# Kernel optimization log

Hardware: AMD Instinct MI355X
Metric: run time of the kernel (lower is better)

The kernel has to match this reference:

```python
import jax, jax.numpy as jnp
import numpy as np

I = 512  # input_size
H = 512  # hidden_size
L = 512  # sequence length
N = 64   # batch


def setup_inputs() -> dict:
    key = jax.random.key(0)
    ks = jax.random.split(key, 12)
    s_ih = 1.0 / np.sqrt(H)
    inp = {
        "input": jax.random.normal(ks[0], (L, N, I), dtype=jnp.float32),
        "h_0": jax.random.normal(ks[1], (2, N, H), dtype=jnp.float32),
        # layer 0 params
        "W_ih_l0": jax.random.uniform(ks[2], (H, I), jnp.float32, -s_ih, s_ih),
        "W_hh_l0": jax.random.uniform(ks[3], (H, H), jnp.float32, -s_ih, s_ih),
        "b_ih_l0": jax.random.uniform(ks[4], (H,), jnp.float32, -s_ih, s_ih),
        "b_hh_l0": jax.random.uniform(ks[5], (H,), jnp.float32, -s_ih, s_ih),
        # layer 1 params (input is layer 0 hidden state, size H)
        "W_ih_l1": jax.random.uniform(ks[6], (H, H), jnp.float32, -s_ih, s_ih),
        "W_hh_l1": jax.random.uniform(ks[7], (H, H), jnp.float32, -s_ih, s_ih),
        "b_ih_l1": jax.random.uniform(ks[8], (H,), jnp.float32, -s_ih, s_ih),
        "b_hh_l1": jax.random.uniform(ks[9], (H,), jnp.float32, -s_ih, s_ih),
    }
    return inp


def reference(input, h_0, W_ih_l0, W_hh_l0, b_ih_l0, b_hh_l0,
              W_ih_l1, W_hh_l1, b_ih_l1, b_hh_l1):
    """2-layer Elman RNN with tanh: h[t] = tanh(x[t] W_ih^T + b_ih + h[t-1] W_hh^T + b_hh).
    Layer 1 consumes layer 0's hidden state at the same timestep.
    Returns (output: (L, N, H), h_n: (2, N, H)).
    """

    def step(carry, x_t):
        h0, h1 = carry  # each (N, H)
        h0_new = jnp.tanh(x_t @ W_ih_l0.T + b_ih_l0 + h0 @ W_hh_l0.T + b_hh_l0)
        h1_new = jnp.tanh(h0_new @ W_ih_l1.T + b_ih_l1 + h1 @ W_hh_l1.T + b_hh_l1)
        return (h0_new, h1_new), h1_new

    (h0_n, h1_n), output = jax.lax.scan(step, (h_0[0], h_0[1]), input)
    h_n = jnp.stack([h0_n, h1_n], axis=0)
    return output, h_n
```

## Files before the change

kernel.cpp:

```cpp
#include <hip/hip_runtime.h>
#include <hip/hip_bf16.h>
#include <math.h>

#define L_SEQ 512
#define N_B   64
#define H_D   512
#define M_TOT (L_SEQ * N_B)

typedef unsigned short u16;
typedef unsigned long long u64;
typedef __attribute__((ext_vector_type(8))) short short8;
typedef __attribute__((ext_vector_type(4))) float f32x4;
typedef __attribute__((ext_vector_type(4))) int i32x4;
typedef __attribute__((ext_vector_type(2))) int i32x2;

__device__ __forceinline__ u16 f2bf(float f) {
    unsigned int u = __builtin_bit_cast(unsigned int, f);
    u = u + 0x7fffu + ((u >> 16) & 1u);
    return (u16)(u >> 16);
}

__device__ __forceinline__ float fast_tanh(float x) {
    float e = __expf(2.0f * x);
    return 1.0f - 2.0f / (e + 1.0f);
}

__device__ __forceinline__ void st_h(u16* p, u16 v) {
    __hip_atomic_store(p, v, __ATOMIC_RELAXED, __HIP_MEMORY_SCOPE_AGENT);
}
__device__ __forceinline__ void st_flag(int* p, int v) {
    __hip_atomic_store(p, v, __ATOMIC_RELAXED, __HIP_MEMORY_SCOPE_AGENT);
}

#define LD16(f, p)                                                          \
  asm volatile(                                                             \
    "global_load_dwordx4 %0, %16, off\n\t"                                  \
    "global_load_dwordx4 %1, %16, off offset:64\n\t"                        \
    "global_load_dwordx4 %2, %16, off offset:128\n\t"                       \
    "global_load_dwordx4 %3, %16, off offset:192\n\t"                       \
    "global_load_dwordx4 %4, %16, off offset:256\n\t"                       \
    "global_load_dwordx4 %5, %16, off offset:320\n\t"                       \
    "global_load_dwordx4 %6, %16, off offset:384\n\t"                       \
    "global_load_dwordx4 %7, %16, off offset:448\n\t"                       \
    "global_load_dwordx4 %8, %16, off offset:512\n\t"                       \
    "global_load_dwordx4 %9, %16, off offset:576\n\t"                       \
    "global_load_dwordx4 %10, %16, off offset:640\n\t"                      \
    "global_load_dwordx4 %11, %16, off offset:704\n\t"                      \
    "global_load_dwordx4 %12, %16, off offset:768\n\t"                      \
    "global_load_dwordx4 %13, %16, off offset:832\n\t"                      \
    "global_load_dwordx4 %14, %16, off offset:896\n\t"                      \
    "global_load_dwordx4 %15, %16, off offset:960\n\t"                      \
    "s_waitcnt vmcnt(0)"                                                    \
    : "=&v"(f[0]), "=&v"(f[1]), "=&v"(f[2]), "=&v"(f[3]),                   \
      "=&v"(f[4]), "=&v"(f[5]), "=&v"(f[6]), "=&v"(f[7]),                   \
      "=&v"(f[8]), "=&v"(f[9]), "=&v"(f[10]), "=&v"(f[11]),                 \
      "=&v"(f[12]), "=&v"(f[13]), "=&v"(f[14]), "=&v"(f[15])                \
    : "v"(p) : "memory")

#define LD16X2(f, g, p0, p1)                                                \
  asm volatile(                                                             \
    "global_load_dwordx4 %0, %32, off\n\t"                                  \
    "global_load_dwordx4 %16, %33, off\n\t"                                 \
    "global_load_dwordx4 %1, %32, off offset:64\n\t"                        \
    "global_load_dwordx4 %17, %33, off offset:64\n\t"                       \
    "global_load_dwordx4 %2, %32, off offset:128\n\t"                       \
    "global_load_dwordx4 %18, %33, off offset:128\n\t"                      \
    "global_load_dwordx4 %3, %32, off offset:192\n\t"                       \
    "global_load_dwordx4 %19, %33, off offset:192\n\t"                      \
    "global_load_dwordx4 %4, %32, off offset:256\n\t"                       \
    "global_load_dwordx4 %20, %33, off offset:256\n\t"                      \
    "global_load_dwordx4 %5, %32, off offset:320\n\t"                       \
    "global_load_dwordx4 %21, %33, off offset:320\n\t"                      \
    "global_load_dwordx4 %6, %32, off offset:384\n\t"                       \
    "global_load_dwordx4 %22, %33, off offset:384\n\t"                      \
    "global_load_dwordx4 %7, %32, off offset:448\n\t"                       \
    "global_load_dwordx4 %23, %33, off offset:448\n\t"                      \
    "global_load_dwordx4 %8, %32, off offset:512\n\t"                       \
    "global_load_dwordx4 %24, %33, off offset:512\n\t"                      \
    "global_load_dwordx4 %9, %32, off offset:576\n\t"                       \
    "global_load_dwordx4 %25, %33, off offset:576\n\t"                      \
    "global_load_dwordx4 %10, %32, off offset:640\n\t"                      \
    "global_load_dwordx4 %26, %33, off offset:640\n\t"                      \
    "global_load_dwordx4 %11, %32, off offset:704\n\t"                      \
    "global_load_dwordx4 %27, %33, off offset:704\n\t"                      \
    "global_load_dwordx4 %12, %32, off offset:768\n\t"                      \
    "global_load_dwordx4 %28, %33, off offset:768\n\t"                      \
    "global_load_dwordx4 %13, %32, off offset:832\n\t"                      \
    "global_load_dwordx4 %29, %33, off offset:832\n\t"                      \
    "global_load_dwordx4 %14, %32, off offset:896\n\t"                      \
    "global_load_dwordx4 %30, %33, off offset:896\n\t"                      \
    "global_load_dwordx4 %15, %32, off offset:960\n\t"                      \
    "global_load_dwordx4 %31, %33, off offset:960\n\t"                      \
    "s_waitcnt vmcnt(0)"                                                    \
    : "=&v"(f[0]), "=&v"(f[1]), "=&v"(f[2]), "=&v"(f[3]),                   \
      "=&v"(f[4]), "=&v"(f[5]), "=&v"(f[6]), "=&v"(f[7]),                   \
      "=&v"(f[8]), "=&v"(f[9]), "=&v"(f[10]), "=&v"(f[11]),                 \
      "=&v"(f[12]), "=&v"(f[13]), "=&v"(f[14]), "=&v"(f[15]),               \
      "=&v"(g[0]), "=&v"(g[1]), "=&v"(g[2]), "=&v"(g[3]),                   \
      "=&v"(g[4]), "=&v"(g[5]), "=&v"(g[6]), "=&v"(g[7]),                   \
      "=&v"(g[8]), "=&v"(g[9]), "=&v"(g[10]), "=&v"(g[11]),                 \
      "=&v"(g[12]), "=&v"(g[13]), "=&v"(g[14]), "=&v"(g[15])                \
    : "v"(p0), "v"(p1) : "memory")

#define WAITVM asm volatile("s_waitcnt vmcnt(0)" ::: "memory")

__global__ void k_prep(const float* __restrict__ x,
                       const float* __restrict__ w0ih, const float* __restrict__ w0hh,
                       const float* __restrict__ b0i,  const float* __restrict__ b0h,
                       const float* __restrict__ w1ih, const float* __restrict__ w1hh,
                       const float* __restrict__ b1i,  const float* __restrict__ b1h,
                       u16* __restrict__ xb,
                       u16* __restrict__ w0ihb, u16* __restrict__ w0hhb,
                       u16* __restrict__ w1ihb, u16* __restrict__ w1hhb,
                       float* __restrict__ bias0, float* __restrict__ bias1,
                       int* __restrict__ flags)
{
    const int stride = gridDim.x * blockDim.x;
    const int tid = blockIdx.x * blockDim.x + threadIdx.x;
    for (int i = tid; i < M_TOT * H_D / 4; i += stride) {
        const float4 v = ((const float4*)x)[i];
        ushort4 o;
        o.x = f2bf(v.x); o.y = f2bf(v.y); o.z = f2bf(v.z); o.w = f2bf(v.w);
        ((ushort4*)xb)[i] = o;
    }
    for (int i = tid; i < H_D * H_D; i += stride) {
        w0ihb[i] = f2bf(w0ih[i]);
        w0hhb[i] = f2bf(w0hh[i]);
        w1ihb[i] = f2bf(w1ih[i]);
        w1hhb[i] = f2bf(w1hh[i]);
    }
    if (tid < H_D) {
        bias0[tid] = b0i[tid] + b0h[tid];
        bias1[tid] = b1i[tid] + b1h[tid];
    }
    if (tid < 192) flags[tid] = 0;
}

__global__ __launch_bounds__(256)
void k_gemm(const u16* __restrict__ A, const u16* __restrict__ W,
            const float* __restrict__ bias, float* __restrict__ out)
{
    __shared__ u16 As[128][40];
    __shared__ u16 Ws[128][40];
    const int m0 = blockIdx.x * 128;
    const int n0 = blockIdx.y * 128;
    const int tid = threadIdx.x;
    const int w = tid >> 6, l = tid & 63, q = l >> 4, lr = l & 15;
    const int mw = (w >> 1) * 64, nw = (w & 1) * 64;
    const int skg = (tid & 3) * 8;
    const int smr = tid >> 2;

    f32x4 acc[4][4];
    #pragma unroll
    for (int i = 0; i < 4; ++i)
        #pragma unroll
        for (int j = 0; j < 4; ++j)
            acc[i][j] = (f32x4){0.f, 0.f, 0.f, 0.f};

    for (int kk = 0; kk < H_D; kk += 32) {
        *(uint4*)&As[smr][skg]      = *(const uint4*)(A + (size_t)(m0 + smr) * H_D + kk + skg);
        *(uint4*)&As[smr + 64][skg] = *(const uint4*)(A + (size_t)(m0 + smr + 64) * H_D + kk + skg);
        *(uint4*)&Ws[smr][skg]      = *(const uint4*)(W + (size_t)(n0 + smr) * H_D + kk + skg);
        *(uint4*)&Ws[smr + 64][skg] = *(const uint4*)(W + (size_t)(n0 + smr + 64) * H_D + kk + skg);
        __syncthreads();
        short8 af[4], bf[4];
        #pragma unroll
        for (int rt = 0; rt < 4; ++rt) af[rt] = *(const short8*)&As[mw + rt*16 + lr][q*8];
        #pragma unroll
        for (int nt = 0; nt < 4; ++nt) bf[nt] = *(const short8*)&Ws[nw + nt*16 + lr][q*8];
        #pragma unroll
        for (int rt = 0; rt < 4; ++rt)
            #pragma unroll
            for (int nt = 0; nt < 4; ++nt)
                acc[rt][nt] = __builtin_amdgcn_mfma_f32_16x16x32_bf16(af[rt], bf[nt], acc[rt][nt], 0, 0, 0);
        __syncthreads();
    }
    #pragma unroll
    for (int nt = 0; nt < 4; ++nt) {
        const int col = n0 + nw + nt*16 + lr;
        const float bv = bias[col];
        #pragma unroll
        for (int rt = 0; rt < 4; ++rt) {
            #pragma unroll
            for (int r = 0; r < 4; ++r) {
                const int row = m0 + mw + rt*16 + q*4 + r;
                out[(size_t)row * H_D + col] = acc[rt][nt][r] + bv;
            }
        }
    }
}

__global__ __launch_bounds__(256, 1)
void k_rec_fused(const u16* __restrict__ Whh0, const u16* __restrict__ Wih1,
                 const u16* __restrict__ Whh1,
                 const float* __restrict__ h_init,
                 const float* __restrict__ pre0,
                 const float* __restrict__ bias1,
                 u16* __restrict__ h0buf, u16* __restrict__ h1buf,
                 float* __restrict__ out, float* __restrict__ hn,
                 int* __restrict__ flags0, int* __restrict__ flags1)
{
    (void)__hip_atomic_load(flags0, __ATOMIC_ACQUIRE, __HIP_MEMORY_SCOPE_AGENT);

    const int tid = threadIdx.x;
    const int w = tid >> 6, l = tid & 63, q = l >> 4, lr = l & 15;
    const int r0 = w * 16;
    const int m = r0 + lr;

    if (blockIdx.x < 16) {
        const int c = blockIdx.x;
        const int nbase = c * 32;
        short8 breg[16][2];
        #pragma unroll
        for (int kt = 0; kt < 16; ++kt)
            #pragma unroll
            for (int nt = 0; nt < 2; ++nt)
                breg[kt][nt] = *(const short8*)(Whh0 + (size_t)(nbase + nt*16 + lr) * H_D + kt*32 + q*8);

        #pragma unroll
        for (int j = 0; j < 8; ++j) {
            int idx = l * 8 + j;
            int row = r0 + (idx >> 5);
            int col = nbase + (idx & 31);
            st_h(h0buf + (size_t)row * H_D + col, f2bf(h_init[row * H_D + col]));
        }
        WAITVM;
        __syncthreads();
        if (tid == 0) st_flag(flags0 + c, 1);

        for (int t = 0; t < L_SEQ; ++t) {
            const float* pt = pre0 + (size_t)t * (N_B * H_D)
                            + (size_t)(r0 + lr) * H_D + nbase + q*4;
            f32x4 acc0a = *(const f32x4*)pt;
            f32x4 acc1a = *(const f32x4*)(pt + 16);
            f32x4 acc0b = (f32x4){0.f,0.f,0.f,0.f};
            f32x4 acc1b = (f32x4){0.f,0.f,0.f,0.f};

            if (w == 0) {
                const int* p = flags0 + (l & 15);
                while (true) {
                    int v = __hip_atomic_load(p, __ATOMIC_RELAXED, __HIP_MEMORY_SCOPE_AGENT);
                    if (__all(v >= t + 1)) break;
                    __builtin_amdgcn_s_sleep(1);
                }
                asm volatile("" ::: "memory");
            }
            __syncthreads();

            const u16* hs = h0buf + ((size_t)t * N_B + m) * H_D + q*8;
            i32x4 f[16];
            LD16(f, hs);
            #pragma unroll
            for (int kt = 0; kt < 16; kt += 2) {
                acc0a = __builtin_amdgcn_mfma_f32_16x16x32_bf16(breg[kt][0],   __builtin_bit_cast(short8, f[kt]),   acc0a, 0, 0, 0);
                acc1a = __builtin_amdgcn_mfma_f32_16x16x32_bf16(breg[kt][1],   __builtin_bit_cast(short8, f[kt]),   acc1a, 0, 0, 0);
                acc0b = __builtin_amdgcn_mfma_f32_16x16x32_bf16(breg[kt+1][0], __builtin_bit_cast(short8, f[kt+1]), acc0b, 0, 0, 0);
                acc1b = __builtin_amdgcn_mfma_f32_16x16x32_bf16(breg[kt+1][1], __builtin_bit_cast(short8, f[kt+1]), acc1b, 0, 0, 0);
            }
            float v0[4], v1[4];
            #pragma unroll
            for (int r = 0; r < 4; ++r) {
                v0[r] = fast_tanh(acc0a[r] + acc0b[r]);
                v1[r] = fast_tanh(acc1a[r] + acc1b[r]);
            }
            i32x2 d0, d1;
            d0[0] = (int)((unsigned)f2bf(v0[0]) | ((unsigned)f2bf(v0[1]) << 16));
            d0[1] = (int)((unsigned)f2bf(v0[2]) | ((unsigned)f2bf(v0[3]) << 16));
            d1[0] = (int)((unsigned)f2bf(v1[0]) | ((unsigned)f2bf(v1[1]) << 16));
            d1[1] = (int)((unsigned)f2bf(v1[2]) | ((unsigned)f2bf(v1[3]) << 16));
            u16* hd = h0buf + (size_t)(t+1) * (N_B * H_D)
                    + (size_t)(r0 + lr) * H_D + nbase + q*4;
            asm volatile(
                "global_store_dwordx2 %2, %0, off sc1\n\t"
                "global_store_dwordx2 %2, %1, off offset:32 sc1"
                :: "v"(d0), "v"(d1), "v"(hd) : "memory");
            WAITVM;
            __syncthreads();
            if (tid == 0) st_flag(flags0 + c, t + 2);

            if (t == L_SEQ - 1) {
                f32x4 o0 = {v0[0], v0[1], v0[2], v0[3]};
                f32x4 o1 = {v1[0], v1[1], v1[2], v1[3]};
                *(f32x4*)(hn + (size_t)(r0 + lr) * H_D + nbase + q*4)      = o0;
                *(f32x4*)(hn + (size_t)(r0 + lr) * H_D + nbase + 16 + q*4) = o1;
            }
        }
    } else {
        const int c = blockIdx.x - 16;
        const int nbase = c * 16;
        short8 bregI[16], bregH[16];
        #pragma unroll
        for (int kt = 0; kt < 16; ++kt) {
            bregI[kt] = *(const short8*)(Wih1 + (size_t)(nbase + lr) * H_D + kt*32 + q*8);
            bregH[kt] = *(const short8*)(Whh1 + (size_t)(nbase + lr) * H_D + kt*32 + q*8);
        }
        const f32x4 bv4 = *(const f32x4*)(bias1 + nbase + q*4);

        const float* hi1 = h_init + N_B * H_D;
        #pragma unroll
        for (int j = 0; j < 4; ++j) {
            int idx = l * 4 + j;
            int row = r0 + (idx >> 4);
            int col = nbase + (idx & 15);
            st_h(h1buf + (size_t)row * H_D + col, f2bf(hi1[row * H_D + col]));
        }
        WAITVM;
        __syncthreads();
        if (tid == 0) st_flag(flags1 + c, 1);

        for (int t = 0; t < L_SEQ; ++t) {
            if (w == 0) {
                const int* p;
                int need;
                if (l < 16)      { p = flags0 + l;        need = t + 2; }
                else if (l < 48) { p = flags1 + (l - 16); need = t + 1; }
                else             { p = flags0;            need = 0;     }
                while (true) {
                    int v = __hip_atomic_load(p, __ATOMIC_RELAXED, __HIP_MEMORY_SCOPE_AGENT);
                    if (__all(v >= need)) break;
                    __builtin_amdgcn_s_sleep(1);
                }
                asm volatile("" ::: "memory");
            }
            __syncthreads();

            const u16* p0 = h0buf + ((size_t)(t+1) * N_B + m) * H_D + q*8;
            const u16* p1 = h1buf + ((size_t)t     * N_B + m) * H_D + q*8;
            i32x4 f[16], g[16];
            LD16X2(f, g, p0, p1);
            f32x4 accA = bv4;
            f32x4 accB = (f32x4){0.f,0.f,0.f,0.f};
            f32x4 accC = (f32x4){0.f,0.f,0.f,0.f};
            f32x4 accD = (f32x4){0.f,0.f,0.f,0.f};
            #pragma unroll
            for (int kt = 0; kt < 16; kt += 2) {
                accA = __builtin_amdgcn_mfma_f32_16x16x32_bf16(bregI[kt],   __builtin_bit_cast(short8, f[kt]),   accA, 0, 0, 0);
                accB = __builtin_amdgcn_mfma_f32_16x16x32_bf16(bregH[kt],   __builtin_bit_cast(short8, g[kt]),   accB, 0, 0, 0);
                accC = __builtin_amdgcn_mfma_f32_16x16x32_bf16(bregI[kt+1], __builtin_bit_cast(short8, f[kt+1]), accC, 0, 0, 0);
                accD = __builtin_amdgcn_mfma_f32_16x16x32_bf16(bregH[kt+1], __builtin_bit_cast(short8, g[kt+1]), accD, 0, 0, 0);
            }
            float v[4];
            #pragma unroll
            for (int r = 0; r < 4; ++r)
                v[r] = fast_tanh(accA[r] + accB[r] + accC[r] + accD[r]);
            i32x2 d;
            d[0] = (int)((unsigned)f2bf(v[0]) | ((unsigned)f2bf(v[1]) << 16));
            d[1] = (int)((unsigned)f2bf(v[2]) | ((unsigned)f2bf(v[3]) << 16));
            u16* hd = h1buf + (size_t)(t+1) * (N_B * H_D)
                    + (size_t)(r0 + lr) * H_D + nbase + q*4;
            asm volatile(
                "global_store_dwordx2 %1, %0, off sc1"
                :: "v"(d), "v"(hd) : "memory");
            WAITVM;
            __syncthreads();
            if (tid == 0) st_flag(flags1 + c, t + 2);

            f32x4 ov = {v[0], v[1], v[2], v[3]};
            *(f32x4*)(out + (size_t)t * (N_B * H_D)
                      + (size_t)(r0 + lr) * H_D + nbase + q*4) = ov;
            if (t == L_SEQ - 1)
                *(f32x4*)(hn + (size_t)(N_B + r0 + lr) * H_D + nbase + q*4) = ov;
        }
    }
}

extern "C" void kernel_launch(void* const* d_in, const int* in_sizes, int n_in,
                              void* d_out, int out_size, void* d_ws, size_t ws_size,
                              hipStream_t stream)
{
    (void)in_sizes; (void)n_in; (void)out_size; (void)ws_size;
    const float* x    = (const float*)d_in[0];
    const float* h0   = (const float*)d_in[1];
    const float* w0ih = (const float*)d_in[2];
    const float* w0hh = (const float*)d_in[3];
    const float* b0i  = (const float*)d_in[4];
    const float* b0h  = (const float*)d_in[5];
    const float* w1ih = (const float*)d_in[6];
    const float* w1hh = (const float*)d_in[7];
    const float* b1i  = (const float*)d_in[8];
    const float* b1h  = (const float*)d_in[9];
    float* out = (float*)d_out;
    float* hn  = out + (size_t)M_TOT * H_D;

    char* ws = (char*)d_ws;
    size_t off = 0;
    u16* w0ihb = (u16*)(ws + off);   off += (size_t)H_D * H_D * 2;
    u16* w0hhb = (u16*)(ws + off);   off += (size_t)H_D * H_D * 2;
    u16* w1ihb = (u16*)(ws + off);   off += (size_t)H_D * H_D * 2;
    u16* w1hhb = (u16*)(ws + off);   off += (size_t)H_D * H_D * 2;
    float* bias0 = (float*)(ws + off); off += H_D * 4;
    float* bias1 = (float*)(ws + off); off += H_D * 4;
    int* flags   = (int*)(ws + off);   off += 256 * 4;
    int* flags0  = flags;
    int* flags1  = flags + 64;
    u16* h0buf   = (u16*)(ws + off);   off += (size_t)(L_SEQ + 1) * N_B * H_D * 2;
    float* pre0  = (float*)(ws + off); off += (size_t)M_TOT * H_D * 4;
    u16* h1buf   = (u16*)(ws + off);   off += (size_t)(L_SEQ + 1) * N_B * H_D * 2;
    u16* xb      = h1buf;

    k_prep<<<2048, 256, 0, stream>>>(x, w0ih, w0hh, b0i, b0h, w1ih, w1hh, b1i, b1h,
                                     xb, w0ihb, w0hhb, w1ihb, w1hhb,
                                     bias0, bias1, flags);
    k_gemm<<<dim3(M_TOT/128, H_D/128), 256, 0, stream>>>(xb, w0ihb, bias0, pre0);
    k_rec_fused<<<48, 256, 0, stream>>>(w0hhb, w1ihb, w1hhb, h0, pre0, bias1,
                                        h0buf, h1buf, out, hn, flags0, flags1);
}
```

Baseline: 3.048 ms.

## Pad sync flags per block, drop spin sleep, permute h0 columns for wide stores

Each block's progress flag now sits in its own 64-byte slot, so the flags no longer share cache lines while other blocks poll them. The s_sleep in the spin-wait loops is removed so waiters see flag updates sooner. The layer-0 hidden-state column order is permuted within 32-column groups, with matching permutations of W_hh_l0 and W_ih_l1 columns and of the initial state, so each lane writes one 16-byte store instead of two 8-byte ones. The MFMA accumulation in layer 0 is also split into four independent chains, which shortens the dependency chain but uses more registers; tight polling also adds memory traffic.

```diff
diff --git a/kernel.cpp b/kernel.cpp
--- a/kernel.cpp
+++ b/kernel.cpp
@@ -31,6 +31,8 @@
 __device__ __forceinline__ void st_flag(int* p, int v) {
     __hip_atomic_store(p, v, __ATOMIC_RELAXED, __HIP_MEMORY_SCOPE_AGENT);
 }
+
+#define FSTRIDE 16
 
 #define LD16(f, p)                                                          \
   asm volatile(                                                             \
@@ -104,6 +106,10 @@
 
 #define WAITVM asm volatile("s_waitcnt vmcnt(0)" ::: "memory")
 
+__device__ __host__ __forceinline__ int perm32(int j) {
+    return (((j >> 3) & 3) << 2) | (j & 3) | (((j >> 2) & 1) << 4);
+}
+
 __global__ void k_prep(const float* __restrict__ x,
                        const float* __restrict__ w0ih, const float* __restrict__ w0hh,
                        const float* __restrict__ b0i,  const float* __restrict__ b0h,
@@ -124,16 +130,18 @@
         ((ushort4*)xb)[i] = o;
     }
     for (int i = tid; i < H_D * H_D; i += stride) {
+        const int p  = i & (H_D - 1);
+        const int pc = (i & ~(H_D - 1)) | (p & ~31) | perm32(p & 31);
         w0ihb[i] = f2bf(w0ih[i]);
-        w0hhb[i] = f2bf(w0hh[i]);
-        w1ihb[i] = f2bf(w1ih[i]);
+        w0hhb[i] = f2bf(w0hh[pc]);
+        w1ihb[i] = f2bf(w1ih[pc]);
         w1hhb[i] = f2bf(w1hh[i]);
     }
     if (tid < H_D) {
         bias0[tid] = b0i[tid] + b0h[tid];
         bias1[tid] = b1i[tid] + b1h[tid];
     }
-    if (tid < 192) flags[tid] = 0;
+    if (tid < 48 * FSTRIDE) flags[tid] = 0;
 }
 
 __global__ __launch_bounds__(256)
@@ -221,12 +229,13 @@
         for (int j = 0; j < 8; ++j) {
             int idx = l * 8 + j;
             int row = r0 + (idx >> 5);
-            int col = nbase + (idx & 31);
-            st_h(h0buf + (size_t)row * H_D + col, f2bf(h_init[row * H_D + col]));
+            int pos = idx & 31;
+            st_h(h0buf + (size_t)row * H_D + nbase + pos,
+                 f2bf(h_init[row * H_D + nbase + perm32(pos)]));
         }
         WAITVM;
         __syncthreads();
-        if (tid == 0) st_flag(flags0 + c, 1);
+        if (tid == 0) st_flag(flags0 + c * FSTRIDE, 1);
 
         for (int t = 0; t < L_SEQ; ++t) {
             const float* pt = pre0 + (size_t)t * (N_B * H_D)
@@ -235,13 +244,16 @@
             f32x4 acc1a = *(const f32x4*)(pt + 16);
             f32x4 acc0b = (f32x4){0.f,0.f,0.f,0.f};
             f32x4 acc1b = (f32x4){0.f,0.f,0.f,0.f};
+            f32x4 acc0c = (f32x4){0.f,0.f,0.f,0.f};
+            f32x4 acc1c = (f32x4){0.f,0.f,0.f,0.f};
+            f32x4 acc0d = (f32x4){0.f,0.f,0.f,0.f};
+            f32x4 acc1d = (f32x4){0.f,0.f,0.f,0.f};
 
             if (w == 0) {
-                const int* p = flags0 + (l & 15);
+                const int* p = flags0 + (l & 15) * FSTRIDE;
                 while (true) {
                     int v = __hip_atomic_load(p, __ATOMIC_RELAXED, __HIP_MEMORY_SCOPE_AGENT);
                     if (__all(v >= t + 1)) break;
-                    __builtin_amdgcn_s_sleep(1);
                 }
                 asm volatile("" ::: "memory");
             }
@@ -251,32 +263,35 @@
             i32x4 f[16];
             LD16(f, hs);
             #pragma unroll
-            for (int kt = 0; kt < 16; kt += 2) {
+            for (int kt = 0; kt < 16; kt += 4) {
                 acc0a = __builtin_amdgcn_mfma_f32_16x16x32_bf16(breg[kt][0],   __builtin_bit_cast(short8, f[kt]),   acc0a, 0, 0, 0);
                 acc1a = __builtin_amdgcn_mfma_f32_16x16x32_bf16(breg[kt][1],   __builtin_bit_cast(short8, f[kt]),   acc1a, 0, 0, 0);
                 acc0b = __builtin_amdgcn_mfma_f32_16x16x32_bf16(breg[kt+1][0], __builtin_bit_cast(short8, f[kt+1]), acc0b, 0, 0, 0);
                 acc1b = __builtin_amdgcn_mfma_f32_16x16x32_bf16(breg[kt+1][1], __builtin_bit_cast(short8, f[kt+1]), acc1b, 0, 0, 0);
+                acc0c = __builtin_amdgcn_mfma_f32_16x16x32_bf16(breg[kt+2][0], __builtin_bit_cast(short8, f[kt+2]), acc0c, 0, 0, 0);
+                acc1c = __builtin_amdgcn_mfma_f32_16x16x32_bf16(breg[kt+2][1], __builtin_bit_cast(short8, f[kt+2]), acc1c, 0, 0, 0);
+                acc0d = __builtin_amdgcn_mfma_f32_16x16x32_bf16(breg[kt+3][0], __builtin_bit_cast(short8, f[kt+3]), acc0d, 0, 0, 0);
+                acc1d = __builtin_amdgcn_mfma_f32_16x16x32_bf16(breg[kt+3][1], __builtin_bit_cast(short8, f[kt+3]), acc1d, 0, 0, 0);
             }
             float v0[4], v1[4];
             #pragma unroll
             for (int r = 0; r < 4; ++r) {
-                v0[r] = fast_tanh(acc0a[r] + acc0b[r]);
-                v1[r] = fast_tanh(acc1a[r] + acc1b[r]);
-            }
-            i32x2 d0, d1;
-            d0[0] = (int)((unsigned)f2bf(v0[0]) | ((unsigned)f2bf(v0[1]) << 16));
-            d0[1] = (int)((unsigned)f2bf(v0[2]) | ((unsigned)f2bf(v0[3]) << 16));
-            d1[0] = (int)((unsigned)f2bf(v1[0]) | ((unsigned)f2bf(v1[1]) << 16));
-            d1[1] = (int)((unsigned)f2bf(v1[2]) | ((unsigned)f2bf(v1[3]) << 16));
+                v0[r] = fast_tanh((acc0a[r] + acc0b[r]) + (acc0c[r] + acc0d[r]));
+                v1[r] = fast_tanh((acc1a[r] + acc1b[r]) + (acc1c[r] + acc1d[r]));
+            }
+            i32x4 dd;
+            dd[0] = (int)((unsigned)f2bf(v0[0]) | ((unsigned)f2bf(v0[1]) << 16));
+            dd[1] = (int)((unsigned)f2bf(v0[2]) | ((unsigned)f2bf(v0[3]) << 16));
+            dd[2] = (int)((unsigned)f2bf(v1[0]) | ((unsigned)f2bf(v1[1]) << 16));
+            dd[3] = (int)((unsigned)f2bf(v1[2]) | ((unsigned)f2bf(v1[3]) << 16));
             u16* hd = h0buf + (size_t)(t+1) * (N_B * H_D)
-                    + (size_t)(r0 + lr) * H_D + nbase + q*4;
+                    + (size_t)(r0 + lr) * H_D + nbase + q*8;
             asm volatile(
-                "global_store_dwordx2 %2, %0, off sc1\n\t"
-                "global_store_dwordx2 %2, %1, off offset:32 sc1"
-                :: "v"(d0), "v"(d1), "v"(hd) : "memory");
+                "global_store_dwordx4 %1, %0, off sc1"
+                :: "v"(dd), "v"(hd) : "memory");
             WAITVM;
             __syncthreads();
-            if (tid == 0) st_flag(flags0 + c, t + 2);
+            if (tid == 0) st_flag(flags0 + c * FSTRIDE, t + 2);
 
             if (t == L_SEQ - 1) {
                 f32x4 o0 = {v0[0], v0[1], v0[2], v0[3]};
@@ -306,19 +321,18 @@
         }
         WAITVM;
         __syncthreads();
-        if (tid == 0) st_flag(flags1 + c, 1);
+        if (tid == 0) st_flag(flags1 + c * FSTRIDE, 1);
 
         for (int t = 0; t < L_SEQ; ++t) {
             if (w == 0) {
                 const int* p;
                 int need;
-                if (l < 16)      { p = flags0 + l;        need = t + 2; }
-                else if (l < 48) { p = flags1 + (l - 16); need = t + 1; }
-                else             { p = flags0;            need = 0;     }
+                if (l < 16)      { p = flags0 + l * FSTRIDE;        need = t + 2; }
+                else if (l < 48) { p = flags1 + (l - 16) * FSTRIDE; need = t + 1; }
+                else             { p = flags0;                      need = 0;     }
                 while (true) {
                     int v = __hip_atomic_load(p, __ATOMIC_RELAXED, __HIP_MEMORY_SCOPE_AGENT);
                     if (__all(v >= need)) break;
-                    __builtin_amdgcn_s_sleep(1);
                 }
                 asm volatile("" ::: "memory");
             }
@@ -342,7 +356,7 @@
             float v[4];
             #pragma unroll
             for (int r = 0; r < 4; ++r)
-                v[r] = fast_tanh(accA[r] + accB[r] + accC[r] + accD[r]);
+                v[r] = fast_tanh((accA[r] + accB[r]) + (accC[r] + accD[r]));
             i32x2 d;
             d[0] = (int)((unsigned)f2bf(v[0]) | ((unsigned)f2bf(v[1]) << 16));
             d[1] = (int)((unsigned)f2bf(v[2]) | ((unsigned)f2bf(v[3]) << 16));
@@ -353,7 +367,7 @@
                 :: "v"(d), "v"(hd) : "memory");
             WAITVM;
             __syncthreads();
-            if (tid == 0) st_flag(flags1 + c, t + 2);
+            if (tid == 0) st_flag(flags1 + c * FSTRIDE, t + 2);
 
             f32x4 ov = {v[0], v[1], v[2], v[3]};
             *(f32x4*)(out + (size_t)t * (N_B * H_D)
@@ -390,9 +404,9 @@
     u16* w1hhb = (u16*)(ws + off);   off += (size_t)H_D * H_D * 2;
     float* bias0 = (float*)(ws + off); off += H_D * 4;
     float* bias1 = (float*)(ws + off); off += H_D * 4;
-    int* flags   = (int*)(ws + off);   off += 256 * 4;
+    int* flags   = (int*)(ws + off);   off += 48 * FSTRIDE * 4;
     int* flags0  = flags;
-    int* flags1  = flags + 64;
+    int* flags1  = flags + 16 * FSTRIDE;
     u16* h0buf   = (u16*)(ws + off);   off += (size_t)(L_SEQ + 1) * N_B * H_D * 2;
     float* pre0  = (float*)(ws + off); off += (size_t)M_TOT * H_D * 4;
     u16* h1buf   = (u16*)(ws + off);   off += (size_t)(L_SEQ + 1) * N_B * H_D * 2;
```

After: 2.935 ms. 3.7% less time.
